# Optimization experiments

Measured on AMD Instinct MI355X. Metric: run time of the kernel, lower is better.

Reference implementation:

```python
import jax, jax.numpy as jnp
import numpy as np

N, I, R, A, O, HEADS, HW, KS = 16, 128, 256, 256, 256, 8, 24, 3
HC = A // HEADS  # head channels
DN = ('NCHW', 'OIHW', 'NCHW')


def _conv(x, w, padding):
    return jax.lax.conv_general_dilated(x, w, (1, 1), padding, dimension_numbers=DN)


def setup_inputs() -> dict:
    key = jax.random.key(0)
    ks = jax.random.split(key, 16)
    g = lambda k, shape, fan: jax.random.normal(k, shape, jnp.float32) * (fan ** -0.5)
    return {
        'x': jax.random.normal(ks[0], (N, I, HW, HW), jnp.float32),
        'h0': jax.random.normal(ks[1], (N, R, HW, HW), jnp.float32) * 0.1,
        'c0': jax.random.normal(ks[2], (N, R, HW, HW), jnp.float32) * 0.1,
        'w_in': g(ks[3], (R, I, 1, 1), I),
        'b_in': jnp.zeros((R,), jnp.float32),
        'wq_x': g(ks[4], (A, R, KS, KS), R * KS * KS * 2 * HC),
        'wq_h': g(ks[5], (A, R, KS, KS), R * KS * KS * 2 * HC),
        'wk_x': g(ks[6], (A, R, KS, KS), R * KS * KS),
        'wk_h': g(ks[7], (A, R, KS, KS), R * KS * KS),
        'wv_x': g(ks[8], (A, R, KS, KS), R * KS * KS * 2),
        'wv_h': g(ks[9], (A, R, KS, KS), R * KS * KS * 2),
        'bv': jnp.zeros((A,), jnp.float32),
        'wg_a': g(ks[10], (4 * R, A, 1, 1), A * 3),
        'bg': jnp.zeros((4 * R,), jnp.float32),
        'wg_x': g(ks[11], (4 * R, R, KS, KS), R * KS * KS * 3),
        'wg_h': g(ks[12], (4 * R, R, KS, KS), R * KS * KS * 3),
        'w_out': g(ks[13], (O, R, 1, 1), R),
        'b_out': jnp.zeros((O,), jnp.float32),
    }


def reference(x, h0, c0, w_in, b_in, wq_x, wq_h, wk_x, wk_h, wv_x, wv_h, bv,
              wg_a, bg, wg_x, wg_h, w_out, b_out):
    # input accumulation (1x1 conv per input, summed; single input here)
    xin = _conv(x, w_in, 'VALID') + b_in[None, :, None, None]  # [N,R,H,W]
    # q: SAME-padded 3x3 convs of x and h (Accumulate = sum)
    q = _conv(xin, wq_x, 'SAME') + _conv(h0, wq_h, 'SAME')      # [N,A,H,W]
    # k, v: VALID 3x3 convs -> spatially reduced key/value positions
    k = _conv(xin, wk_x, 'VALID') + _conv(h0, wk_h, 'VALID')    # [N,A,H-2,W-2]
    v = _conv(xin, wv_x, 'VALID') + _conv(h0, wv_h, 'VALID') + bv[None, :, None, None]
    Q = HW * HW
    D = (HW - KS + 1) * (HW - KS + 1)
    qh = q.reshape(N, HEADS, HC, Q)
    kh = k.reshape(N, HEADS, HC, D)
    vh = v.reshape(N, HEADS, HC, D)
    w = jax.nn.softmax(jnp.einsum('ngcq,ngcd->ngqd', qh, kh), axis=-1)  # [N,G,Q,D]
    a = jnp.einsum('ngcd,ngqd->ngcq', vh, w).reshape(N, A, HW, HW)
    # fused i,f,g,o gate projections: 1x1 conv on a + 3x3 SAME convs on x and h
    gates = (_conv(a, wg_a, 'VALID') + bg[None, :, None, None]
             + _conv(xin, wg_x, 'SAME') + _conv(h0, wg_h, 'SAME'))      # [N,4R,H,W]
    i, f, gg, o = jnp.split(gates, 4, axis=1)
    c = jax.nn.sigmoid(f) * c0 + jax.nn.sigmoid(i) * jnp.tanh(gg)
    h = jax.nn.sigmoid(o) * jnp.tanh(c)
    return _conv(h, w_out, 'VALID') + b_out[None, :, None, None]
```

## Files before the change

kernel.cpp:

```cpp
#include <hip/hip_runtime.h>
#include <cstddef>

constexpr int kN  = 16;
constexpr int kI  = 128;
constexpr int kHW = 24;
constexpr int kQ  = 576;
constexpr int kD  = 484;
constexpr int kDP = 512;
constexpr int kPP = 676;

constexpr int kKTQKV = 144;
constexpr int kKTG   = 152;
constexpr int kKTO   = 8;

constexpr size_t H_XPAD   = 0;
constexpr size_t H_HPAD   = 2768896;
constexpr size_t H_APQKV  = 5537792;
constexpr size_t H_APG    = 9076736;
constexpr size_t H_APO    = 14057472;
constexpr size_t H_A16    = 14123008;
constexpr size_t H_H16    = 16482304;
constexpr size_t H_Q16C   = 18841600;
constexpr size_t H_KT16   = 21200896;
constexpr size_t H_VC16   = 23298048;

using half8    = __attribute__((ext_vector_type(8))) _Float16;
using floatx16 = __attribute__((ext_vector_type(16))) float;

__device__ __forceinline__ float sigm(float x) { return 1.0f / (1.0f + __expf(-x)); }
__device__ __forceinline__ float tanh_f(float x) {
    float e = __expf(2.0f * fabsf(x));
    float r = 1.0f - 2.0f / (e + 1.0f);
    return copysignf(r, x);
}
__device__ __forceinline__ half8 LD8(const _Float16* p) { return *(const half8*)p; }
__device__ __forceinline__ void ST8(_Float16* p, half8 v) { *(half8*)p = v; }


__global__ void pack_qkv_kernel(const float* __restrict__ wq_x, const float* __restrict__ wq_h,
                                const float* __restrict__ wk_x, const float* __restrict__ wk_h,
                                const float* __restrict__ wv_x, const float* __restrict__ wv_h,
                                _Float16* __restrict__ dst) {
    int pidx = blockIdx.x * 256 + threadIdx.x;
    int j = pidx & 7, row = (pidx >> 3) & 127, hl = (pidx >> 10) & 1, kk = (pidx >> 11) & 1;
    int tile = pidx >> 12;
    int mt = tile / kKTQKV, kt = tile - mt * kKTQKV;
    int m = mt * 128 + row;
    int k = kt * 32 + kk * 16 + hl * 8 + j;
    int srcs = (k >= 2304) ? 1 : 0;
    int r = k - srcs * 2304;
    int tap = r >> 8, ic = r & 255;
    const float* w; int mm;
    if (m < 256)      { w = srcs ? wq_h : wq_x; mm = m; }
    else if (m < 512) { w = srcs ? wk_h : wk_x; mm = m - 256; }
    else              { w = srcs ? wv_h : wv_x; mm = m - 512; }
    dst[pidx] = (_Float16)w[((size_t)mm * 256 + ic) * 9 + tap];
}

__global__ void pack_gates_kernel(const float* __restrict__ wg_x, const float* __restrict__ wg_h,
                                  const float* __restrict__ wg_a, _Float16* __restrict__ dst) {
    int pidx = blockIdx.x * 256 + threadIdx.x;
    int j = pidx & 7, row = (pidx >> 3) & 127, hl = (pidx >> 10) & 1, kk = (pidx >> 11) & 1;
    int tile = pidx >> 12;
    int mt = tile / kKTG, kt = tile - mt * kKTG;
    int P = mt * 128 + row;
    int T = P >> 5, ch_local = (P >> 2) & 7, g = P & 3;
    int m = g * 256 + T * 8 + ch_local;
    int k = kt * 32 + kk * 16 + hl * 8 + j;
    float val;
    if (k < 4608) {
        int srcs = (k >= 2304) ? 1 : 0;
        int r = k - srcs * 2304;
        int tap = r >> 8, ic = r & 255;
        const float* w = srcs ? wg_h : wg_x;
        val = w[((size_t)m * 256 + ic) * 9 + tap];
    } else {
        val = wg_a[(size_t)m * 256 + (k - 4608)];
    }
    dst[pidx] = (_Float16)val;
}

__global__ void pack_out_kernel(const float* __restrict__ src, _Float16* __restrict__ dst) {
    int pidx = blockIdx.x * 256 + threadIdx.x;
    int j = pidx & 7, row = (pidx >> 3) & 127, hl = (pidx >> 10) & 1, kk = (pidx >> 11) & 1;
    int tile = pidx >> 12;
    int mt = tile >> 3, kt = tile & 7;
    int m = mt * 128 + row;
    int k = kt * 32 + kk * 16 + hl * 8 + j;
    dst[pidx] = (_Float16)src[(size_t)m * 256 + k];
}

__global__ void pad_nhwc_kernel(const float* __restrict__ src, _Float16* __restrict__ dst) {
    __shared__ float tile[32][65];
    int pxt = blockIdx.x, ict = blockIdx.y, n = blockIdx.z;
    int tid = threadIdx.x;
    {
        int icl = tid >> 6, pxl = tid & 63;
        #pragma unroll
        for (int rep = 0; rep < 8; ++rep) {
            int ic = ict * 32 + rep * 4 + icl;
            tile[rep * 4 + icl][pxl] = src[((size_t)n * 256 + ic) * kQ + pxt * 64 + pxl];
        }
    }
    __syncthreads();
    {
        int icl = tid & 31, pxl0 = tid >> 5;
        #pragma unroll
        for (int rep = 0; rep < 8; ++rep) {
            int pxl = rep * 8 + pxl0;
            int px = pxt * 64 + pxl;
            int y = px / kHW, x = px - y * kHW;
            dst[((size_t)n * kPP + (size_t)(y + 1) * 26 + (x + 1)) * 256 + ict * 32 + icl] =
                (_Float16)tile[icl][pxl];
        }
    }
}

__global__ void conv1x1_pad_kernel(const float* __restrict__ x, const float* __restrict__ w,
                                   const float* __restrict__ b, _Float16* __restrict__ out) {
    int px = blockIdx.x * 64 + threadIdx.x;
    int n = blockIdx.z;
    int oc0 = __builtin_amdgcn_readfirstlane(blockIdx.y * 16 + threadIdx.y * 4);
    const float* ip = x + (size_t)n * kI * kQ + px;
    float acc[4] = {0.f, 0.f, 0.f, 0.f};
    #pragma unroll 4
    for (int ic = 0; ic < kI; ++ic) {
        float xv = ip[(size_t)ic * kQ];
        #pragma unroll
        for (int j = 0; j < 4; ++j) acc[j] = fmaf(xv, w[(size_t)(oc0 + j) * kI + ic], acc[j]);
    }
    int y = px / kHW, xc = px - y * kHW;
    _Float16* op = out + ((size_t)n * kPP + (size_t)(y + 1) * 26 + (xc + 1)) * 256 + oc0;
    #pragma unroll
    for (int j = 0; j < 4; ++j) op[j] = (_Float16)(acc[j] + b[oc0 + j]);
}

template<int BMODE, int EMODE>
__global__ __launch_bounds__(256)
void gemm_kernel(const _Float16* __restrict__ Apack,
                 const _Float16* __restrict__ B1, const _Float16* __restrict__ B2,
                 const _Float16* __restrict__ B3,
                 _Float16* __restrict__ q16, _Float16* __restrict__ k16,
                 _Float16* __restrict__ v16, _Float16* __restrict__ h16,
                 const float* __restrict__ c0, float* __restrict__ outf,
                 const float* __restrict__ bias, int Ktiles, int Ktot) {
    __shared__ _Float16 Bs[2][2560];
    const int tid = threadIdx.x;
    const int wv = tid >> 6, lane = tid & 63, l31 = lane & 31, hl = lane >> 5;
    const int nt = blockIdx.x, mt = blockIdx.y, n = blockIdx.z;

    floatx16 acc0 = {}, acc1 = {};

    const _Float16* aptr = Apack + (size_t)mt * Ktiles * 4096
                         + (size_t)hl * 1024 + (size_t)(wv * 32 + l31) * 8;

    const int px_l = tid >> 2, bc = tid & 3;
    const int px = nt * 64 + px_l;
    const int by = px / kHW, bx = px - by * kHW;
    const int wofs = px_l * 40 + bc * 8;
    const int r0 = l31 * 40 + hl * 8;

    for (int kt = 0; kt < Ktiles; ++kt) {
        const _Float16* bp;
        if (BMODE == 2 && kt >= 144) {
            bp = B3 + ((size_t)n * kQ + px) * 256 + (kt - 144) * 32 + bc * 8;
        } else if (BMODE == 0 || BMODE == 2) {
            int srcs = (kt >= 72) ? 1 : 0;
            int t2 = kt - srcs * 72;
            int tap = t2 >> 3, ict = t2 & 7;
            int ty = (tap * 11) >> 5;
            int tx = tap - ty * 3;
            const _Float16* img = srcs ? B2 : B1;
            bp = img + ((size_t)n * kPP + (size_t)(by + ty) * 26 + (bx + tx)) * 256
                     + ict * 32 + bc * 8;
        } else {
            bp = B1 + ((size_t)n * kQ + px) * Ktot + kt * 32 + bc * 8;
        }
        half8 bv = LD8(bp);
        half8 a0 = LD8(aptr);
        half8 a1 = LD8(aptr + 2048);
        aptr += 4096;
        ST8(&Bs[kt & 1][wofs], bv);
        __syncthreads();
        const _Float16* bb = Bs[kt & 1];
        half8 b00 = LD8(bb + r0);
        half8 b01 = LD8(bb + r0 + 1280);
        half8 b10 = LD8(bb + r0 + 16);
        half8 b11 = LD8(bb + r0 + 1296);
        acc0 = __builtin_amdgcn_mfma_f32_32x32x16_f16(a0, b00, acc0, 0, 0, 0);
        acc1 = __builtin_amdgcn_mfma_f32_32x32x16_f16(a0, b01, acc1, 0, 0, 0);
        acc0 = __builtin_amdgcn_mfma_f32_32x32x16_f16(a1, b10, acc0, 0, 0, 0);
        acc1 = __builtin_amdgcn_mfma_f32_32x32x16_f16(a1, b11, acc1, 0, 0, 0);
        __syncthreads();
    }

    #pragma unroll
    for (int ntile = 0; ntile < 2; ++ntile) {
        const floatx16& A = ntile ? acc1 : acc0;
        const int pxe = nt * 64 + ntile * 32 + l31;
        if (EMODE == 0) {
            const int mrow = mt * 128 + wv * 32;
            if (mrow < 256) {
                #pragma unroll
                for (int r = 0; r < 16; ++r) {
                    int rowi = (r & 3) + 8 * (r >> 2) + 4 * hl;
                    q16[((size_t)n * 256 + mrow + rowi) * kQ + pxe] = (_Float16)A[r];
                }
            } else {
                int yy = pxe / kHW, xx = pxe - yy * kHW;
                if (yy >= 1 && yy <= 22 && xx >= 1 && xx <= 22) {
                    int d = (yy - 1) * 22 + (xx - 1);
                    #pragma unroll
                    for (int r = 0; r < 16; ++r) {
                        int ch = (mrow & 255) + (r & 3) + 8 * (r >> 2) + 4 * hl;
                        int head = n * 8 + (ch >> 5);
                        if (mrow < 512)
                            k16[((size_t)head * kDP + d) * 32 + (ch & 31)] = (_Float16)A[r];
                        else
                            v16[((size_t)head * 32 + (ch & 31)) * kDP + d] =
                                (_Float16)(A[r] + bias[ch]);
                    }
                }
            }
        } else if (EMODE == 3) {
            const int T = mt * 4 + wv;
            #pragma unroll
            for (int q4 = 0; q4 < 4; ++q4) {
                int c = T * 8 + 2 * q4 + hl;
                float iv = A[4 * q4 + 0] + bias[c];
                float fv = A[4 * q4 + 1] + bias[256 + c];
                float gv = A[4 * q4 + 2] + bias[512 + c];
                float ov = A[4 * q4 + 3] + bias[768 + c];
                float c0v = c0[((size_t)n * 256 + c) * kQ + pxe];
                float cn = sigm(fv) * c0v + sigm(iv) * tanh_f(gv);
                h16[((size_t)n * kQ + pxe) * 256 + c] = (_Float16)(sigm(ov) * tanh_f(cn));
            }
        } else {
            const int mrow = mt * 128 + wv * 32;
            #pragma unroll
            for (int r = 0; r < 16; ++r) {
                int m = mrow + (r & 3) + 8 * (r >> 2) + 4 * hl;
                outf[((size_t)n * 256 + m) * kQ + pxe] = A[r] + bias[m];
            }
        }
    }
}

__global__ __launch_bounds__(128)
void attn_kernel(const _Float16* __restrict__ q16c, const _Float16* __restrict__ kT16,
                 const _Float16* __restrict__ vC16, _Float16* __restrict__ a16) {
    const int lane = threadIdx.x & 63;
    const int wv   = threadIdx.x >> 6;
    const int l31 = lane & 31, hl = lane >> 5;
    const int head = blockIdx.y;
    const int n = head >> 3, hd = head & 7;
    const int qt = blockIdx.x * 2 + wv;
    const int q0 = qt * 32;

    half8 qf0, qf1;
    {
        const _Float16* qb = q16c + ((size_t)n * 256 + hd * 32 + hl * 8) * kQ + q0 + l31;
        #pragma unroll
        for (int j = 0; j < 8; ++j) {
            qf0[j] = qb[(size_t)j * kQ];
            qf1[j] = qb[(size_t)(16 + j) * kQ];
        }
    }

    const _Float16* kbase0 = kT16 + ((size_t)head * kDP + l31) * 32 + hl * 8;
    const _Float16* vbase0 = vC16 + ((size_t)head * 32 + l31) * kDP + hl * 8;

    floatx16 acc = {};
    float m_run = -1e30f, l_run = 0.f;

    half8 kf0 = LD8(kbase0);
    half8 kf1 = LD8(kbase0 + 16);

    for (int dt = 0; dt < 16; ++dt) {
        const int d0 = dt * 32;
        floatx16 S = {};
        S = __builtin_amdgcn_mfma_f32_32x32x16_f16(kf0, qf0, S, 0, 0, 0);
        S = __builtin_amdgcn_mfma_f32_32x32x16_f16(kf1, qf1, S, 0, 0, 0);

        half8 vf0 = LD8(vbase0 + d0);
        half8 vf1 = LD8(vbase0 + d0 + 16);
        if (dt < 15) {
            kf0 = LD8(kbase0 + (size_t)(d0 + 32) * 32);
            kf1 = LD8(kbase0 + (size_t)(d0 + 32) * 32 + 16);
        }

        if (dt == 15) {
            #pragma unroll
            for (int r = 0; r < 16; ++r)
                if (!(hl == 0 && r < 4)) S[r] = -1e30f;
        }

        float tmax = S[0];
        #pragma unroll
        for (int r = 1; r < 16; ++r) tmax = fmaxf(tmax, S[r]);
        tmax = fmaxf(tmax, __shfl_xor(tmax, 32));
        float mnew = fmaxf(m_run, tmax);
        float f = __expf(m_run - mnew);
        float p[16], psum = 0.f;
        #pragma unroll
        for (int r = 0; r < 16; ++r) { p[r] = __expf(S[r] - mnew); psum += p[r]; }
        psum += __shfl_xor(psum, 32);
        l_run = f * l_run + psum;
        #pragma unroll
        for (int r = 0; r < 16; ++r) acc[r] *= f;
        m_run = mnew;

        float other[16];
        #pragma unroll
        for (int r = 0; r < 16; ++r) other[r] = __shfl_xor(p[r], 32);
        half8 pf0, pf1;
        #pragma unroll
        for (int t = 0; t < 4; ++t) {
            pf0[t]     = (_Float16)(hl ? other[4 + t]  : p[t]);
            pf0[4 + t] = (_Float16)(hl ? p[4 + t]      : other[t]);
            pf1[t]     = (_Float16)(hl ? other[12 + t] : p[8 + t]);
            pf1[4 + t] = (_Float16)(hl ? p[12 + t]     : other[8 + t]);
        }

        acc = __builtin_amdgcn_mfma_f32_32x32x16_f16(vf0, pf0, acc, 0, 0, 0);
        acc = __builtin_amdgcn_mfma_f32_32x32x16_f16(vf1, pf1, acc, 0, 0, 0);
    }

    float inv = 1.f / l_run;
    _Float16* ap = a16 + ((size_t)n * kQ + q0 + l31) * 256 + hd * 32;
    #pragma unroll
    for (int r = 0; r < 16; ++r) {
        int c = (r & 3) + 8 * (r >> 2) + 4 * hl;
        ap[c] = (_Float16)(acc[r] * inv);
    }
}

extern "C" void kernel_launch(void* const* d_in, const int* in_sizes, int n_in,
                              void* d_out, int out_size, void* d_ws, size_t ws_size,
                              hipStream_t stream) {
    (void)in_sizes; (void)n_in; (void)out_size; (void)ws_size;
    const float* x     = (const float*)d_in[0];
    const float* h0    = (const float*)d_in[1];
    const float* c0    = (const float*)d_in[2];
    const float* w_in  = (const float*)d_in[3];
    const float* b_in  = (const float*)d_in[4];
    const float* wq_x  = (const float*)d_in[5];
    const float* wq_h  = (const float*)d_in[6];
    const float* wk_x  = (const float*)d_in[7];
    const float* wk_h  = (const float*)d_in[8];
    const float* wv_x  = (const float*)d_in[9];
    const float* wv_h  = (const float*)d_in[10];
    const float* bv    = (const float*)d_in[11];
    const float* wg_a  = (const float*)d_in[12];
    const float* bg    = (const float*)d_in[13];
    const float* wg_x  = (const float*)d_in[14];
    const float* wg_h  = (const float*)d_in[15];
    const float* w_out = (const float*)d_in[16];
    const float* b_out = (const float*)d_in[17];

    _Float16* wh = (_Float16*)d_ws;
    _Float16* xpad16  = wh + H_XPAD;
    _Float16* hpad16  = wh + H_HPAD;
    _Float16* apqkv   = wh + H_APQKV;
    _Float16* apg     = wh + H_APG;
    _Float16* apo     = wh + H_APO;
    _Float16* a16     = wh + H_A16;
    _Float16* h16     = wh + H_H16;
    _Float16* q16c    = wh + H_Q16C;
    _Float16* kT16    = wh + H_KT16;
    _Float16* vC16    = wh + H_VC16;

    hipMemsetAsync(wh, 0, 11075584, stream);

    pack_qkv_kernel<<<13824, 256, 0, stream>>>(wq_x, wq_h, wk_x, wk_h, wv_x, wv_h, apqkv);
    pack_gates_kernel<<<19456, 256, 0, stream>>>(wg_x, wg_h, wg_a, apg);
    pack_out_kernel<<<256, 256, 0, stream>>>(w_out, apo);

    pad_nhwc_kernel<<<dim3(9, 8, kN), 256, 0, stream>>>(h0, hpad16);
    conv1x1_pad_kernel<<<dim3(9, 16, kN), dim3(64, 4), 0, stream>>>(x, w_in, b_in, xpad16);

    gemm_kernel<0, 0><<<dim3(9, 6, kN), 256, 0, stream>>>(
        apqkv, xpad16, hpad16, nullptr, q16c, kT16, vC16, nullptr,
        nullptr, nullptr, bv, kKTQKV, 0);

    attn_kernel<<<dim3(9, 128), 128, 0, stream>>>(q16c, kT16, vC16, a16);

    gemm_kernel<2, 3><<<dim3(9, 8, kN), 256, 0, stream>>>(
        apg, xpad16, hpad16, a16, nullptr, nullptr, nullptr, h16,
        c0, nullptr, bg, kKTG, 0);

    gemm_kernel<1, 2><<<dim3(9, 2, kN), 256, 0, stream>>>(
        apo, h16, nullptr, nullptr, nullptr, nullptr, nullptr, nullptr,
        nullptr, (float*)d_out, b_out, kKTO, 256);
}
```

Baseline: 509.9 us.

## Software-pipeline GEMM main loop with register prefetch and a single barrier per tile

The GEMM K-loop is restructured so that global loads of the A and B fragments for tile k+2 are issued into registers before the MFMAs of tile k run. The loop is unrolled by two, with a ping-pong shared-memory buffer. Each tile now takes one __syncthreads instead of two, and global-load latency overlaps with matrix-core work. The cost is higher register pressure, and the loop assumes an even number of K tiles.

```diff
diff --git a/kernel.cpp b/kernel.cpp
--- a/kernel.cpp
+++ b/kernel.cpp
@@ -151,8 +151,8 @@
 
     floatx16 acc0 = {}, acc1 = {};
 
-    const _Float16* aptr = Apack + (size_t)mt * Ktiles * 4096
-                         + (size_t)hl * 1024 + (size_t)(wv * 32 + l31) * 8;
+    const _Float16* abase = Apack + (size_t)mt * Ktiles * 4096
+                          + hl * 1024 + (size_t)(wv * 32 + l31) * 8;
 
     const int px_l = tid >> 2, bc = tid & 3;
     const int px = nt * 64 + px_l;
@@ -160,38 +160,69 @@
     const int wofs = px_l * 40 + bc * 8;
     const int r0 = l31 * 40 + hl * 8;
 
-    for (int kt = 0; kt < Ktiles; ++kt) {
-        const _Float16* bp;
-        if (BMODE == 2 && kt >= 144) {
-            bp = B3 + ((size_t)n * kQ + px) * 256 + (kt - 144) * 32 + bc * 8;
-        } else if (BMODE == 0 || BMODE == 2) {
+    auto bptr = [&](int kt) -> const _Float16* {
+        if (BMODE == 2 && kt >= 144)
+            return B3 + ((size_t)n * kQ + px) * 256 + (kt - 144) * 32 + bc * 8;
+        if (BMODE == 0 || BMODE == 2) {
             int srcs = (kt >= 72) ? 1 : 0;
             int t2 = kt - srcs * 72;
             int tap = t2 >> 3, ict = t2 & 7;
             int ty = (tap * 11) >> 5;
             int tx = tap - ty * 3;
             const _Float16* img = srcs ? B2 : B1;
-            bp = img + ((size_t)n * kPP + (size_t)(by + ty) * 26 + (bx + tx)) * 256
-                     + ict * 32 + bc * 8;
-        } else {
-            bp = B1 + ((size_t)n * kQ + px) * Ktot + kt * 32 + bc * 8;
-        }
-        half8 bv = LD8(bp);
-        half8 a0 = LD8(aptr);
-        half8 a1 = LD8(aptr + 2048);
-        aptr += 4096;
-        ST8(&Bs[kt & 1][wofs], bv);
-        __syncthreads();
-        const _Float16* bb = Bs[kt & 1];
-        half8 b00 = LD8(bb + r0);
-        half8 b01 = LD8(bb + r0 + 1280);
-        half8 b10 = LD8(bb + r0 + 16);
-        half8 b11 = LD8(bb + r0 + 1296);
-        acc0 = __builtin_amdgcn_mfma_f32_32x32x16_f16(a0, b00, acc0, 0, 0, 0);
-        acc1 = __builtin_amdgcn_mfma_f32_32x32x16_f16(a0, b01, acc1, 0, 0, 0);
-        acc0 = __builtin_amdgcn_mfma_f32_32x32x16_f16(a1, b10, acc0, 0, 0, 0);
-        acc1 = __builtin_amdgcn_mfma_f32_32x32x16_f16(a1, b11, acc1, 0, 0, 0);
-        __syncthreads();
+            return img + ((size_t)n * kPP + (size_t)(by + ty) * 26 + (bx + tx)) * 256
+                       + ict * 32 + bc * 8;
+        }
+        return B1 + ((size_t)n * kQ + px) * Ktot + kt * 32 + bc * 8;
+    };
+
+    half8 bq0 = LD8(bptr(0));
+    half8 bq1 = LD8(bptr(1));
+    half8 aq0[2], aq1[2];
+    aq0[0] = LD8(abase);          aq0[1] = LD8(abase + 2048);
+    aq1[0] = LD8(abase + 4096);   aq1[1] = LD8(abase + 4096 + 2048);
+    ST8(&Bs[0][wofs], bq0);
+    __syncthreads();
+
+    for (int kt = 0; kt < Ktiles; kt += 2) {
+        {
+            const _Float16* bb = Bs[0];
+            half8 b00 = LD8(bb + r0);
+            half8 b01 = LD8(bb + r0 + 1280);
+            half8 b10 = LD8(bb + r0 + 16);
+            half8 b11 = LD8(bb + r0 + 1296);
+            half8 a0 = aq0[0], a1 = aq0[1];
+            if (kt + 2 < Ktiles) {
+                bq0 = LD8(bptr(kt + 2));
+                const _Float16* ap = abase + (size_t)(kt + 2) * 4096;
+                aq0[0] = LD8(ap);  aq0[1] = LD8(ap + 2048);
+            }
+            acc0 = __builtin_amdgcn_mfma_f32_32x32x16_f16(a0, b00, acc0, 0, 0, 0);
+            acc1 = __builtin_amdgcn_mfma_f32_32x32x16_f16(a0, b01, acc1, 0, 0, 0);
+            acc0 = __builtin_amdgcn_mfma_f32_32x32x16_f16(a1, b10, acc0, 0, 0, 0);
+            acc1 = __builtin_amdgcn_mfma_f32_32x32x16_f16(a1, b11, acc1, 0, 0, 0);
+            ST8(&Bs[1][wofs], bq1);
+            __syncthreads();
+        }
+        {
+            const _Float16* bb = Bs[1];
+            half8 b00 = LD8(bb + r0);
+            half8 b01 = LD8(bb + r0 + 1280);
+            half8 b10 = LD8(bb + r0 + 16);
+            half8 b11 = LD8(bb + r0 + 1296);
+            half8 a0 = aq1[0], a1 = aq1[1];
+            if (kt + 3 < Ktiles) {
+                bq1 = LD8(bptr(kt + 3));
+                const _Float16* ap = abase + (size_t)(kt + 3) * 4096;
+                aq1[0] = LD8(ap);  aq1[1] = LD8(ap + 2048);
+            }
+            acc0 = __builtin_amdgcn_mfma_f32_32x32x16_f16(a0, b00, acc0, 0, 0, 0);
+            acc1 = __builtin_amdgcn_mfma_f32_32x32x16_f16(a0, b01, acc1, 0, 0, 0);
+            acc0 = __builtin_amdgcn_mfma_f32_32x32x16_f16(a1, b10, acc0, 0, 0, 0);
+            acc1 = __builtin_amdgcn_mfma_f32_32x32x16_f16(a1, b11, acc1, 0, 0, 0);
+            if (kt + 2 < Ktiles) ST8(&Bs[0][wofs], bq0);
+            __syncthreads();
+        }
     }
 
     #pragma unroll
```

Measured after the change: 499.7 us. -2.0%, faster.

## Pipeline GEMM B-tile loads via direct global-to-LDS with two K-tiles per step

Applied to the files above, without the earlier changes.

The conv-GEMM main loop now issues B-operand loads with global_load_lds directly into a double-buffered shared tile and prefetches the A fragments one step ahead. Each iteration covers two K-tiles, which halves the barrier count. The grid is flattened so batch and pixel tile share blockIdx.x. The aim is to hide global latency behind the MFMAs and cut synchronisation. The trade-off is that the unpadded LDS layout (stride 32 instead of 40) may bank-conflict, and the code relies on the async LDS writes being visible after the barrier.

```diff
diff --git a/kernel.cpp b/kernel.cpp
--- a/kernel.cpp
+++ b/kernel.cpp
@@ -35,6 +35,12 @@
 }
 __device__ __forceinline__ half8 LD8(const _Float16* p) { return *(const half8*)p; }
 __device__ __forceinline__ void ST8(_Float16* p, half8 v) { *(half8*)p = v; }
+
+__device__ __forceinline__ void glds16(const _Float16* g, _Float16* l) {
+    __builtin_amdgcn_global_load_lds(
+        (const __attribute__((address_space(1))) void*)g,
+        (__attribute__((address_space(3))) void*)l, 16, 0, 0);
+}
 
 
 __global__ void pack_qkv_kernel(const float* __restrict__ wq_x, const float* __restrict__ wq_h,
@@ -144,53 +150,82 @@
                  _Float16* __restrict__ v16, _Float16* __restrict__ h16,
                  const float* __restrict__ c0, float* __restrict__ outf,
                  const float* __restrict__ bias, int Ktiles, int Ktot) {
-    __shared__ _Float16 Bs[2][2560];
+    __shared__ _Float16 Bs[2][4096];
     const int tid = threadIdx.x;
     const int wv = tid >> 6, lane = tid & 63, l31 = lane & 31, hl = lane >> 5;
-    const int nt = blockIdx.x, mt = blockIdx.y, n = blockIdx.z;
+    const int bxid = blockIdx.x;
+    const int n = bxid / 9, nt = bxid - n * 9;
+    const int mt = blockIdx.y;
 
     floatx16 acc0 = {}, acc1 = {};
 
-    const _Float16* aptr = Apack + (size_t)mt * Ktiles * 4096
-                         + (size_t)hl * 1024 + (size_t)(wv * 32 + l31) * 8;
-
-    const int px_l = tid >> 2, bc = tid & 3;
+    const _Float16* abase = Apack + (size_t)mt * Ktiles * 4096
+                          + hl * 1024 + (size_t)(wv * 32 + l31) * 8;
+
+    const int px_l = wv * 16 + (lane >> 2);
+    const int bc = lane & 3;
     const int px = nt * 64 + px_l;
-    const int by = px / kHW, bx = px - by * kHW;
-    const int wofs = px_l * 40 + bc * 8;
-    const int r0 = l31 * 40 + hl * 8;
-
-    for (int kt = 0; kt < Ktiles; ++kt) {
-        const _Float16* bp;
-        if (BMODE == 2 && kt >= 144) {
-            bp = B3 + ((size_t)n * kQ + px) * 256 + (kt - 144) * 32 + bc * 8;
-        } else if (BMODE == 0 || BMODE == 2) {
+    const int by = px / kHW, bxp = px - by * kHW;
+    _Float16* ldsw0 = &Bs[0][wv * 512];
+    _Float16* ldsw1 = &Bs[1][wv * 512];
+
+    auto gaddr = [&](int kt) -> const _Float16* {
+        if (BMODE == 2 && kt >= 144)
+            return B3 + ((size_t)n * kQ + px) * 256 + (kt - 144) * 32 + bc * 8;
+        if (BMODE == 0 || BMODE == 2) {
             int srcs = (kt >= 72) ? 1 : 0;
             int t2 = kt - srcs * 72;
             int tap = t2 >> 3, ict = t2 & 7;
             int ty = (tap * 11) >> 5;
             int tx = tap - ty * 3;
             const _Float16* img = srcs ? B2 : B1;
-            bp = img + ((size_t)n * kPP + (size_t)(by + ty) * 26 + (bx + tx)) * 256
-                     + ict * 32 + bc * 8;
-        } else {
-            bp = B1 + ((size_t)n * kQ + px) * Ktot + kt * 32 + bc * 8;
-        }
-        half8 bv = LD8(bp);
-        half8 a0 = LD8(aptr);
-        half8 a1 = LD8(aptr + 2048);
-        aptr += 4096;
-        ST8(&Bs[kt & 1][wofs], bv);
-        __syncthreads();
-        const _Float16* bb = Bs[kt & 1];
+            return img + ((size_t)n * kPP + (size_t)(by + ty) * 26 + (bxp + tx)) * 256
+                       + ict * 32 + bc * 8;
+        }
+        return B1 + ((size_t)n * kQ + px) * Ktot + kt * 32 + bc * 8;
+    };
+
+    const int steps = Ktiles >> 1;
+
+    glds16(gaddr(0), ldsw0);
+    glds16(gaddr(1), ldsw0 + 2048);
+    half8 aq0 = LD8(abase);
+    half8 aq1 = LD8(abase + 2048);
+    half8 aq2 = LD8(abase + 4096);
+    half8 aq3 = LD8(abase + 4096 + 2048);
+    __syncthreads();
+
+    for (int s = 0; s < steps; ++s) {
+        const int buf = s & 1;
+        if (s + 1 < steps) {
+            _Float16* ld = buf ? ldsw0 : ldsw1;
+            glds16(gaddr(2 * s + 2), ld);
+            glds16(gaddr(2 * s + 3), ld + 2048);
+        }
+        half8 a0 = aq0, a1 = aq1, a2 = aq2, a3 = aq3;
+        if (s + 1 < steps) {
+            const _Float16* ap = abase + (size_t)(2 * s + 2) * 4096;
+            aq0 = LD8(ap);          aq1 = LD8(ap + 2048);
+            aq2 = LD8(ap + 4096);   aq3 = LD8(ap + 4096 + 2048);
+        }
+        const _Float16* bb = Bs[buf];
+        const int r0 = l31 * 32 + hl * 8;
         half8 b00 = LD8(bb + r0);
-        half8 b01 = LD8(bb + r0 + 1280);
+        half8 b01 = LD8(bb + r0 + 1024);
         half8 b10 = LD8(bb + r0 + 16);
-        half8 b11 = LD8(bb + r0 + 1296);
+        half8 b11 = LD8(bb + r0 + 1040);
         acc0 = __builtin_amdgcn_mfma_f32_32x32x16_f16(a0, b00, acc0, 0, 0, 0);
         acc1 = __builtin_amdgcn_mfma_f32_32x32x16_f16(a0, b01, acc1, 0, 0, 0);
         acc0 = __builtin_amdgcn_mfma_f32_32x32x16_f16(a1, b10, acc0, 0, 0, 0);
         acc1 = __builtin_amdgcn_mfma_f32_32x32x16_f16(a1, b11, acc1, 0, 0, 0);
+        half8 c00 = LD8(bb + 2048 + r0);
+        half8 c01 = LD8(bb + 2048 + r0 + 1024);
+        half8 c10 = LD8(bb + 2048 + r0 + 16);
+        half8 c11 = LD8(bb + 2048 + r0 + 1040);
+        acc0 = __builtin_amdgcn_mfma_f32_32x32x16_f16(a2, c00, acc0, 0, 0, 0);
+        acc1 = __builtin_amdgcn_mfma_f32_32x32x16_f16(a2, c01, acc1, 0, 0, 0);
+        acc0 = __builtin_amdgcn_mfma_f32_32x32x16_f16(a3, c10, acc0, 0, 0, 0);
+        acc1 = __builtin_amdgcn_mfma_f32_32x32x16_f16(a3, c11, acc1, 0, 0, 0);
         __syncthreads();
     }
 
@@ -379,17 +414,17 @@
     pad_nhwc_kernel<<<dim3(9, 8, kN), 256, 0, stream>>>(h0, hpad16);
     conv1x1_pad_kernel<<<dim3(9, 16, kN), dim3(64, 4), 0, stream>>>(x, w_in, b_in, xpad16);
 
-    gemm_kernel<0, 0><<<dim3(9, 6, kN), 256, 0, stream>>>(
+    gemm_kernel<0, 0><<<dim3(144, 6), 256, 0, stream>>>(
         apqkv, xpad16, hpad16, nullptr, q16c, kT16, vC16, nullptr,
         nullptr, nullptr, bv, kKTQKV, 0);
 
     attn_kernel<<<dim3(9, 128), 128, 0, stream>>>(q16c, kT16, vC16, a16);
 
-    gemm_kernel<2, 3><<<dim3(9, 8, kN), 256, 0, stream>>>(
+    gemm_kernel<2, 3><<<dim3(144, 8), 256, 0, stream>>>(
         apg, xpad16, hpad16, a16, nullptr, nullptr, nullptr, h16,
         c0, nullptr, bg, kKTG, 0);
 
-    gemm_kernel<1, 2><<<dim3(9, 2, kN), 256, 0, stream>>>(
+    gemm_kernel<1, 2><<<dim3(144, 2), 256, 0, stream>>>(
         apo, h16, nullptr, nullptr, nullptr, nullptr, nullptr, nullptr,
         nullptr, (float*)d_out, b_out, kKTO, 256);
 }
```

Measured after the change: 473.5 us. 7.1% less time.
